# Performance work log

Hardware: AMD Instinct MI355X
Metric: run time of the kernel (lower is better)

Reference implementation:

```python
import jax, jax.numpy as jnp
import numpy as np

N0, N1, N2 = 2000, 6000, 4000
C = 128
T = 2  # conv_order
N_LAYERS = 2


def _cheb(L, x):
    """Chebyshev-style repeated application: returns [n, c, T]."""
    outs = []
    cur = x
    for _ in range(T):
        cur = L @ cur
        outs.append(cur)
    return jnp.stack(outs, axis=-1)


def _sccnn_layer(x0, x1, x2, L0, L1d, L1u, L2d, L2u, B1, B2, w0, w1, w2):
    # node space
    x_0_to_0 = jnp.concatenate([x0[..., None], _cheb(L0, x0)], -1)          # [N0,C,1+T]
    x_1_to_0 = B1 @ x1
    x_1_to_0 = jnp.concatenate([x_1_to_0[..., None], _cheb(L0, x_1_to_0)], -1)
    x_0_all = jnp.concatenate([x_0_to_0, x_1_to_0], -1)                      # [N0,C,2T+2]

    # edge space
    x_1_to_1 = jnp.concatenate([x1[..., None], _cheb(L1d, x1), _cheb(L1u, x1)], -1)  # [N1,C,2T+1]
    x_0_to_1 = B1.T @ x0
    x_0_to_1 = jnp.concatenate([x_0_to_1[..., None], _cheb(L1d, x_0_to_1)], -1)
    x_2_to_1 = B2 @ x2
    x_2_to_1 = jnp.concatenate([x_2_to_1[..., None], _cheb(L1u, x_2_to_1)], -1)
    x_1_all = jnp.concatenate([x_1_to_1, x_0_to_1, x_2_to_1], -1)            # [N1,C,4T+3]

    # face space (sc_order > 2: down+up Laplacians)
    x_2_to_2 = jnp.concatenate([x2[..., None], _cheb(L2d, x2), _cheb(L2u, x2)], -1)
    x_1_to_2 = B2.T @ x1
    x_1_to_2 = jnp.concatenate([x_1_to_2[..., None], _cheb(L2d, x_1_to_2)], -1)
    x_2_all = jnp.concatenate([x_2_to_2, x_1_to_2], -1)                      # [N2,C,3T+2]

    y0 = jnp.einsum("nik,iok->no", x_0_all, w0)
    y1 = jnp.einsum("nik,iok->no", x_1_all, w1)
    y2 = jnp.einsum("nik,iok->no", x_2_all, w2)
    return y0, y1, y2  # update_func=None


def setup_inputs() -> dict:
    key = jax.random.key(0)
    ks = jax.random.split(key, 32)
    f32 = jnp.float32
    inp = {
        "x0": jax.random.normal(ks[0], (N0, C), f32),
        "x1": jax.random.normal(ks[1], (N1, C), f32),
        "x2": jax.random.normal(ks[2], (N2, C), f32),
        # scale operators ~1/sqrt(n) so repeated application stays well-conditioned
        "L0": jax.random.normal(ks[3], (N0, N0), f32) / np.float32(N0) ** 0.5,
        "L1d": jax.random.normal(ks[4], (N1, N1), f32) / np.float32(N1) ** 0.5,
        "L1u": jax.random.normal(ks[5], (N1, N1), f32) / np.float32(N1) ** 0.5,
        "L2d": jax.random.normal(ks[6], (N2, N2), f32) / np.float32(N2) ** 0.5,
        "L2u": jax.random.normal(ks[7], (N2, N2), f32) / np.float32(N2) ** 0.5,
        "B1": jax.random.normal(ks[8], (N0, N1), f32) / np.float32(N1) ** 0.5,
        "B2": jax.random.normal(ks[9], (N1, N2), f32) / np.float32(N2) ** 0.5,
        # input linears (torch Linear: y = x @ W.T + b, W:[out,in])
        "in_w0": jax.random.normal(ks[10], (C, C), f32) * 0.05,
        "in_b0": jnp.zeros((C,), f32),
        "in_w1": jax.random.normal(ks[11], (C, C), f32) * 0.05,
        "in_b1": jnp.zeros((C,), f32),
        "in_w2": jax.random.normal(ks[12], (C, C), f32) * 0.05,
        "in_b2": jnp.zeros((C,), f32),
        # layer 0 weights: [in, out, k]
        "l0_w0": jax.random.normal(ks[13], (C, C, 2 * T + 2), f32) * 0.05,
        "l0_w1": jax.random.normal(ks[14], (C, C, 4 * T + 3), f32) * 0.05,
        "l0_w2": jax.random.normal(ks[15], (C, C, 3 * T + 2), f32) * 0.05,
        # layer 1 weights
        "l1_w0": jax.random.normal(ks[16], (C, C, 2 * T + 2), f32) * 0.05,
        "l1_w1": jax.random.normal(ks[17], (C, C, 4 * T + 3), f32) * 0.05,
        "l1_w2": jax.random.normal(ks[18], (C, C, 3 * T + 2), f32) * 0.05,
        # output linear on nodes -> 2 classes
        "out_w": jax.random.normal(ks[19], (2, C), f32) * 0.05,
        "out_b": jnp.zeros((2,), f32),
    }
    return inp


def reference(x0, x1, x2, L0, L1d, L1u, L2d, L2u, B1, B2,
              in_w0, in_b0, in_w1, in_b1, in_w2, in_b2,
              l0_w0, l0_w1, l0_w2, l1_w0, l1_w1, l1_w2,
              out_w, out_b):
    h0 = x0 @ in_w0.T + in_b0
    h1 = x1 @ in_w1.T + in_b1
    h2 = x2 @ in_w2.T + in_b2
    layer_ws = [(l0_w0, l0_w1, l0_w2), (l1_w0, l1_w1, l1_w2)]
    for w0, w1, w2 in layer_ws:
        h0, h1, h2 = _sccnn_layer(h0, h1, h2, L0, L1d, L1u, L2d, L2u, B1, B2, w0, w1, w2)
    logits = h0 @ out_w.T + out_b  # [N0, 2]
    return jax.nn.sigmoid(logits)
```

## Files before the change

### kernel.cpp

```cpp
#include <hip/hip_runtime.h>
#include <cstdint>

typedef __bf16 bf16_t;
typedef bf16_t bf16x8 __attribute__((ext_vector_type(8)));
typedef float f32x4v __attribute__((ext_vector_type(4)));
typedef float f32x16 __attribute__((ext_vector_type(16)));
typedef unsigned long long u64;

#define GLD16(gp, lp)                                                        \
  __builtin_amdgcn_global_load_lds(                                          \
      (const __attribute__((address_space(1))) unsigned int*)(gp),           \
      (__attribute__((address_space(3))) unsigned int*)(lp), 16, 0, 0)

struct GDesc {
  const void* A; const void* Ac; const void* Bt; const void* Bc; const void* bias;
  bf16_t* outN; bf16_t* outT;
  int M, N, K, lda, ldbt, ldN, ldT, bstart, nbm, aext, bext;
};
struct GBatch { const unsigned* flagp; int nd; GDesc d[6]; };

__device__ __forceinline__ int imin(int a, int b) { return a < b ? a : b; }

__global__ __launch_bounds__(256) void detect_dtype(const void* probe, unsigned* flag) {
  __shared__ int cnt;
  if (threadIdx.x == 0) cnt = 0;
  __syncthreads();
  const unsigned short* u = (const unsigned short*)probe;
  int c = 0;
  for (int i = threadIdx.x; i < 4096; i += 256) {
    int e = (u[2 * i] >> 7) & 0xFF;
    if (e >= 97 && e <= 157) c++;
  }
  atomicAdd(&cnt, c);
  __syncthreads();
  if (threadIdx.x == 0) *flag = (cnt >= 3277) ? 1u : 0u;
}

struct CvtJob { const float* src; bf16_t* dst; };
struct CvtBatch {
  const unsigned* flagp; int nj; unsigned total4;
  unsigned base[12]; CvtJob j[12];
};
__global__ __launch_bounds__(256) void cvt_f32_bf16(CvtBatch cb) {
  if (*cb.flagp != 0) return;
  const unsigned stride = gridDim.x * 256;
  for (unsigned idx = blockIdx.x * 256 + threadIdx.x; idx < cb.total4; idx += stride) {
    int ji = 0;
#pragma unroll 1
    for (int i = 1; i < cb.nj; ++i)
      if (idx >= cb.base[i]) ji = i;
    const unsigned e = idx - cb.base[ji];
    float4 v = ((const float4*)cb.j[ji].src)[e];
    union { bf16_t b[4]; uint2 u; } o;
    o.b[0] = (bf16_t)v.x; o.b[1] = (bf16_t)v.y;
    o.b[2] = (bf16_t)v.z; o.b[3] = (bf16_t)v.w;
    *(uint2*)(cb.j[ji].dst + (u64)e * 4) = o.u;
  }
}

__global__ __launch_bounds__(256) void gemm_stage(GBatch gb) {
  __shared__ __align__(16) char smem[49152];
  bf16_t* const sAb = (bf16_t*)smem;
  bf16_t* const sBb = (bf16_t*)smem + 3 * 4096;
  float* const sT = (float*)smem;

  const int bid = blockIdx.x;
  int di = 0;
#pragma unroll 1
  for (int i = 1; i < gb.nd; ++i)
    if (bid >= gb.d[i].bstart) di = i;
  const GDesc g = gb.d[di];

  const unsigned fl = *gb.flagp;
  bool a32 = false, b32 = false;
  const bf16_t* Ab; const bf16_t* Bb;
  const float* Af = (const float*)g.A;
  const float* Bf = (const float*)g.Bt;
  if (fl != 0) {
    Ab = (const bf16_t*)g.A; Bb = (const bf16_t*)g.Bt;
  } else {
    if (g.aext) { Ab = (const bf16_t*)g.Ac; a32 = (g.Ac == nullptr); }
    else Ab = (const bf16_t*)g.A;
    if (g.bext) { Bb = (const bf16_t*)g.Bc; b32 = (g.Bc == nullptr); }
    else Bb = (const bf16_t*)g.Bt;
  }

  const int t = threadIdx.x;
  const int w = t >> 6, lane = t & 63;
  const int local = bid - g.bstart;
  const int bm = local % g.nbm, bn = local / g.nbm;
  const int m0 = bm * 128, c0 = bn * 128;

  const int srow = t >> 2;
  const int sc = ((t & 3) ^ ((t >> 3) & 3)) * 8;
  const u64 eA0 = (u64)imin(m0 + srow, g.M - 1) * g.lda + sc;
  const u64 eA1 = (u64)imin(m0 + 64 + srow, g.M - 1) * g.lda + sc;
  const u64 eB0 = (u64)imin(c0 + srow, g.N - 1) * g.ldbt + sc;
  const u64 eB1 = (u64)imin(c0 + 64 + srow, g.N - 1) * g.ldbt + sc;

  const int wm = w & 1, wn = w >> 1;
  const int lrow = lane & 31, lhalf = lane >> 5;
  const int fr = (lrow >> 1) & 3;
  const int aoffb = (wm * 64 + lrow) * 32;
  const int boffb = (wn * 64 + lrow) * 32;

  f32x16 acc[2][2] = {};

  auto cvt8 = [](const float* p) {
    float4 u0 = *(const float4*)p, u1 = *(const float4*)(p + 4);
    bf16x8 r;
    r[0] = (bf16_t)u0.x; r[1] = (bf16_t)u0.y; r[2] = (bf16_t)u0.z; r[3] = (bf16_t)u0.w;
    r[4] = (bf16_t)u1.x; r[5] = (bf16_t)u1.y; r[6] = (bf16_t)u1.z; r[7] = (bf16_t)u1.w;
    return r;
  };

  auto mfma_step = [&](const bf16_t* bA, const bf16_t* bB) {
    bf16x8 af[2][2], bb[2][2];
#pragma unroll
    for (int s = 0; s < 2; ++s)
#pragma unroll
      for (int h = 0; h < 2; ++h) {
        const int sl = ((lhalf + 2 * h) ^ fr) * 8;
        af[s][h] = *(const bf16x8*)&bA[aoffb + s * 1024 + sl];
        bb[s][h] = *(const bf16x8*)&bB[boffb + s * 1024 + sl];
      }
#pragma unroll
    for (int h = 0; h < 2; ++h)
#pragma unroll
      for (int sm = 0; sm < 2; ++sm)
#pragma unroll
        for (int sn = 0; sn < 2; ++sn)
          acc[sm][sn] = __builtin_amdgcn_mfma_f32_32x32x16_bf16(
              af[sm][h], bb[sn][h], acc[sm][sn], 0, 0, 0);
  };

  auto issueP = [&](int kk, int buf) {
    const u64 kb = (u64)kk * 32;
    bf16_t* dA = sAb + buf * 4096 + w * 512;
    bf16_t* dB = sBb + buf * 4096 + w * 512;
    GLD16(Ab + eA0 + kb, dA);
    GLD16(Ab + eA1 + kb, dA + 2048);
    GLD16(Bb + eB0 + kb, dB);
    GLD16(Bb + eB1 + kb, dB + 2048);
  };

  const int kfull = g.K >> 5;
  if (!a32 && !b32) {
    issueP(0, 0);
    if (kfull > 1) {
      issueP(1, 1);
      asm volatile("s_waitcnt vmcnt(4)" ::: "memory");
    } else {
      asm volatile("s_waitcnt vmcnt(0)" ::: "memory");
    }
    __builtin_amdgcn_s_barrier();
    int cur = 0, nxt = 2;
#pragma unroll 1
    for (int kk = 0; kk < kfull; ++kk) {
      const bool pre = (kk + 2 < kfull);
      if (pre) issueP(kk + 2, nxt);
      mfma_step(sAb + cur * 4096, sBb + cur * 4096);
      if (pre) asm volatile("s_waitcnt vmcnt(4)" ::: "memory");
      else     asm volatile("s_waitcnt vmcnt(0)" ::: "memory");
      __builtin_amdgcn_s_barrier();
      cur = (cur == 2) ? 0 : cur + 1;
      nxt = (nxt == 2) ? 0 : nxt + 1;
    }
  } else {
#pragma unroll 1
    for (int kk = 0; kk < kfull; ++kk) {
      const u64 kb = (u64)kk * 32;
      if (!a32) {
        GLD16(Ab + eA0 + kb, sAb + w * 512);
        GLD16(Ab + eA1 + kb, sAb + w * 512 + 2048);
      } else {
        *(bf16x8*)(sAb + (u64)t * 8) = cvt8(Af + eA0 + kb);
        *(bf16x8*)(sAb + (u64)t * 8 + 2048) = cvt8(Af + eA1 + kb);
      }
      if (!b32) {
        GLD16(Bb + eB0 + kb, sBb + w * 512);
        GLD16(Bb + eB1 + kb, sBb + w * 512 + 2048);
      } else {
        *(bf16x8*)(sBb + (u64)t * 8) = cvt8(Bf + eB0 + kb);
        *(bf16x8*)(sBb + (u64)t * 8 + 2048) = cvt8(Bf + eB1 + kb);
      }
      __syncthreads();
      mfma_step(sAb, sBb);
      __syncthreads();
    }
  }

  if (g.K & 16) {
    const u64 k0 = (u64)(g.K & ~31);
    const int row = t >> 1;
    const int g0 = t & 1;
    const int ftl = (row >> 1) & 3;
    const u64 ea = (u64)imin(m0 + row, g.M - 1) * g.lda + k0 + g0 * 8;
    const u64 eb = (u64)imin(c0 + row, g.N - 1) * g.ldbt + k0 + g0 * 8;
    bf16x8 va, vb;
    if (!a32) va = *(const bf16x8*)(Ab + ea);
    else va = cvt8(Af + ea);
    if (!b32) vb = *(const bf16x8*)(Bb + eb);
    else vb = cvt8(Bf + eb);
    uint4 z = {0, 0, 0, 0};
    *(bf16x8*)&sAb[row * 32 + ((g0 ^ ftl) * 8)] = va;
    *(uint4*)&sAb[row * 32 + (((g0 | 2) ^ ftl) * 8)] = z;
    *(bf16x8*)&sBb[row * 32 + ((g0 ^ ftl) * 8)] = vb;
    *(uint4*)&sBb[row * 32 + (((g0 | 2) ^ ftl) * 8)] = z;
    __syncthreads();
    mfma_step(sAb, sBb);
    __syncthreads();
  }

  if (g.bias) {
#pragma unroll
    for (int sm = 0; sm < 2; ++sm)
#pragma unroll
      for (int reg = 0; reg < 16; ++reg) {
        int mg = imin(m0 + wm * 64 + sm * 32 + (reg & 3) + 8 * (reg >> 2) + 4 * lhalf,
                      g.M - 1);
        float bv = (fl == 0) ? ((const float*)g.bias)[mg]
                             : (float)((const bf16_t*)g.bias)[mg];
        acc[sm][0][reg] += bv;
        acc[sm][1][reg] += bv;
      }
  }
  if (g.outN) {
#pragma unroll
    for (int sm = 0; sm < 2; ++sm)
#pragma unroll
      for (int sn = 0; sn < 2; ++sn) {
        int cg = c0 + wn * 64 + sn * 32 + lrow;
        if (cg < g.N) {
#pragma unroll
          for (int reg = 0; reg < 16; ++reg) {
            int mg = m0 + wm * 64 + sm * 32 + (reg & 3) + 8 * (reg >> 2) + 4 * lhalf;
            if (mg < g.M) g.outN[(u64)mg * g.ldN + cg] = (bf16_t)acc[sm][sn][reg];
          }
        }
      }
  }
  if (g.outT) {
#pragma unroll
    for (int cc = 0; cc < 4; ++cc) {
      __syncthreads();
      if (wn == (cc >> 1)) {
        const int sn = cc & 1;
#pragma unroll
        for (int sm = 0; sm < 2; ++sm)
#pragma unroll
          for (int rq = 0; rq < 4; ++rq) {
            f32x4v v;
            v.x = acc[sm][sn][rq * 4 + 0];
            v.y = acc[sm][sn][rq * 4 + 1];
            v.z = acc[sm][sn][rq * 4 + 2];
            v.w = acc[sm][sn][rq * 4 + 3];
            int ml = wm * 64 + sm * 32 + 8 * rq + 4 * lhalf;
            *(f32x4v*)&sT[lrow * 132 + ml] = v;
          }
      }
      __syncthreads();
#pragma unroll
      for (int p = 0; p < 4; ++p) {
        int c = (t >> 5) + p * 8, mq = t & 31;
        f32x4v v = *(const f32x4v*)&sT[c * 132 + mq * 4];
        int cg = c0 + cc * 32 + c;
        if (cg < g.N) {
          union { bf16_t b[4]; uint2 u; } cv;
          cv.b[0] = (bf16_t)v.x; cv.b[1] = (bf16_t)v.y;
          cv.b[2] = (bf16_t)v.z; cv.b[3] = (bf16_t)v.w;
          *(uint2*)(g.outT + (u64)cg * g.ldT + m0 + mq * 4) = cv.u;
        }
      }
    }
  }
}

__global__ __launch_bounds__(256) void transpose_any(const void* in, bf16_t* out,
                                                     bf16_t* out_rm,
                                                     int Ri, int Ci, int tilesC,
                                                     const unsigned* flagp) {
  __shared__ bf16_t tile[64 * 65];
  const bool f32m = (*flagp == 0);
  const int bi = blockIdx.x / tilesC, bj = blockIdx.x % tilesC;
  const int i0 = bi * 64, j0 = bj * 64;
  const int t = threadIdx.x;
#pragma unroll
  for (int it = 0; it < 16; ++it) {
    int flidx = t + it * 256;
    int r = flidx >> 6, c = flidx & 63;
    int gi = i0 + r, gj = j0 + c;
    bf16_t v = (bf16_t)0.f;
    if (gi < Ri && gj < Ci) {
      u64 idx = (u64)gi * Ci + gj;
      v = f32m ? (bf16_t)((const float*)in)[idx] : ((const bf16_t*)in)[idx];
      if (out_rm && f32m) out_rm[idx] = v;
    }
    tile[r * 65 + c] = v;
  }
  __syncthreads();
#pragma unroll
  for (int it = 0; it < 2; ++it) {
    int flidx = t + it * 256;
    int c = flidx >> 3, rb = (flidx & 7) * 8;
    int gj = j0 + c;
    if (gj < Ci && (i0 + rb) < Ri) {
      union { bf16_t b[8]; uint4 u; } cv;
#pragma unroll
      for (int k2 = 0; k2 < 8; ++k2) cv.b[k2] = tile[(rb + k2) * 65 + c];
      *(uint4*)(out + (u64)gj * Ri + i0 + rb) = cv.u;
    }
  }
}

struct RPack {
  const void* src[3]; bf16_t* dst[3];
  int R[3], ks[3], base[3], total;
  const unsigned* flagp;
};
__global__ __launch_bounds__(256) void repack_w(RPack rp) {
  int id = blockIdx.x * 256 + threadIdx.x;
  if (id >= rp.total) return;
  const bool f32m = (*rp.flagp == 0);
  int si = 0;
  if (id >= rp.base[1]) si = 1;
  if (id >= rp.base[2]) si = 2;
  int e = id - rp.base[si];
  int R = rp.R[si], ks = rp.ks[si];
  int o = e / R, col = e - o * R;
  int k = col >> 7, i = col & 127;
  u64 sidx = ((u64)i * 128 + o) * ks + k;
  rp.dst[si][e] = f32m ? (bf16_t)((const float*)rp.src[si])[sidx]
                       : ((const bf16_t*)rp.src[si])[sidx];
}

__global__ __launch_bounds__(256) void final_head(const bf16_t* h0t, const void* ow,
                                                  const void* ob, void* out,
                                                  const unsigned* flagp) {
  int n = blockIdx.x * 256 + threadIdx.x;
  if (n >= 2000) return;
  const bool f32m = (*flagp == 0);
  float a0 = f32m ? ((const float*)ob)[0] : (float)((const bf16_t*)ob)[0];
  float a1 = f32m ? ((const float*)ob)[1] : (float)((const bf16_t*)ob)[1];
#pragma unroll 4
  for (int i = 0; i < 128; ++i) {
    float hv = (float)h0t[i * 2048 + n];
    float w0 = f32m ? ((const float*)ow)[i] : (float)((const bf16_t*)ow)[i];
    float w1 = f32m ? ((const float*)ow)[128 + i] : (float)((const bf16_t*)ow)[128 + i];
    a0 += hv * w0;
    a1 += hv * w1;
  }
  float s0 = 1.f / (1.f + __expf(-a0));
  float s1 = 1.f / (1.f + __expf(-a1));
  if (f32m) {
    ((float*)out)[n * 2 + 0] = s0;
    ((float*)out)[n * 2 + 1] = s1;
  } else {
    ((bf16_t*)out)[n * 2 + 0] = (bf16_t)s0;
    ((bf16_t*)out)[n * 2 + 1] = (bf16_t)s1;
  }
}

extern "C" void kernel_launch(void* const* d_in, const int* in_sizes, int n_in,
                              void* d_out, int out_size, void* d_ws, size_t ws_size,
                              hipStream_t stream) {
  const void *x0 = d_in[0], *x1 = d_in[1], *x2 = d_in[2];
  const void *L0 = d_in[3], *L1d = d_in[4], *L1u = d_in[5];
  const void *B1m = d_in[8];
  const void *B2m = d_in[9];
  const void *inw0 = d_in[10], *inb0 = d_in[11], *inw1 = d_in[12], *inb1 = d_in[13],
             *inw2 = d_in[14], *inb2 = d_in[15];
  const void *w0a = d_in[16], *w1a = d_in[17], *w0b = d_in[19];
  const void *outw = d_in[22], *outb = d_in[23];

  char* wsb = (char*)d_ws;
  size_t off = 0;
  auto alloc = [&](size_t elems) {
    bf16_t* p = (bf16_t*)(wsb + off);
    off = (off + elems * 2 + 255) & ~(size_t)255;
    return p;
  };
  unsigned* flagp = (unsigned*)alloc(128);
  bf16_t* B1t = alloc((size_t)6000 * 2000);
  bf16_t* h0t = alloc(128 * 2048);
  bf16_t* h1t = alloc(128 * 6016);
  bf16_t* h2t = alloc(128 * 4096);
  bf16_t* p_t = alloc(128 * 2048);
  bf16_t* q_t = alloc(128 * 6016);
  bf16_t* r_t = alloc(128 * 6016);
  bf16_t* a_t = alloc(128 * 2048);
  bf16_t* c_t = alloc(128 * 2048);
  bf16_t* e_t = alloc(128 * 6016);
  bf16_t* g_t = alloc(128 * 6016);
  bf16_t* j_t = alloc(128 * 6016);
  bf16_t* l_t = alloc(128 * 6016);
  bf16_t* sA0 = alloc((size_t)2000 * 768);
  bf16_t* sA1 = alloc((size_t)6000 * 1408);
  bf16_t* sB0 = alloc((size_t)2000 * 768);
  bf16_t* Wp0a = alloc(768 * 128);
  bf16_t* Wp1a = alloc(1408 * 128);
  bf16_t* Wp0b = alloc(768 * 128);
  bf16_t* L0c  = alloc((size_t)2000 * 2000);
  bf16_t* L1dc = alloc((size_t)6000 * 6000);
  bf16_t* L1uc = alloc((size_t)6000 * 6000);
  bf16_t* B2c  = alloc((size_t)6000 * 4000);
  bf16_t* B1rm = alloc((size_t)2000 * 6000);
  bf16_t* x0c  = alloc((size_t)2000 * 128);
  bf16_t* x1c  = alloc((size_t)6000 * 128);
  bf16_t* x2c  = alloc((size_t)4000 * 128);
  bf16_t* iw0c = alloc(128 * 128);
  bf16_t* iw1c = alloc(128 * 128);
  bf16_t* iw2c = alloc(128 * 128);

  const bool fit = off <= ws_size;
  auto C = [&](bf16_t* p) { return fit ? p : (bf16_t*)nullptr; };

  detect_dtype<<<1, 256, 0, stream>>>(L0, flagp);

  if (fit) {
    CvtBatch cb{};
    cb.flagp = flagp;
    int nj = 0; unsigned tot4 = 0;
    auto addcvt = [&](const void* src, bf16_t* dst, size_t n) {
      cb.j[nj].src = (const float*)src; cb.j[nj].dst = dst;
      cb.base[nj] = tot4; tot4 += (unsigned)(n >> 2); nj++;
    };
    addcvt(L0, L0c, (size_t)2000 * 2000);
    addcvt(L1d, L1dc, (size_t)6000 * 6000);
    addcvt(L1u, L1uc, (size_t)6000 * 6000);
    addcvt(B2m, B2c, (size_t)6000 * 4000);
    addcvt(x0, x0c, (size_t)2000 * 128);
    addcvt(x1, x1c, (size_t)6000 * 128);
    addcvt(x2, x2c, (size_t)4000 * 128);
    addcvt(inw0, iw0c, 128 * 128);
    addcvt(inw1, iw1c, 128 * 128);
    addcvt(inw2, iw2c, 128 * 128);
    cb.nj = nj; cb.total4 = tot4;
    cvt_f32_bf16<<<2048, 256, 0, stream>>>(cb);
  }

  RPack rp{};
  rp.src[0] = w0a; rp.dst[0] = Wp0a; rp.R[0] = 768;  rp.ks[0] = 6;  rp.base[0] = 0;
  rp.src[1] = w1a; rp.dst[1] = Wp1a; rp.R[1] = 1408; rp.ks[1] = 11; rp.base[1] = 98304;
  rp.src[2] = w0b; rp.dst[2] = Wp0b; rp.R[2] = 768;  rp.ks[2] = 6;  rp.base[2] = 98304 + 180224;
  rp.total = 98304 + 180224 + 98304;
  rp.flagp = flagp;
  repack_w<<<(rp.total + 255) / 256, 256, 0, stream>>>(rp);

  transpose_any<<<32 * 94, 256, 0, stream>>>(B1m, B1t, C(B1rm), 2000, 6000, 94, flagp);

  GBatch gb; int tot;
  gb.flagp = flagp;
  auto reset = [&] { gb.nd = 0; tot = 0; };
  auto add = [&](const void* A, const void* Ac, int aext,
                 const void* Bt, const void* Bc, int bext, const void* bias,
                 bf16_t* outN, int ldN, bf16_t* outT, int ldT,
                 int M, int N, int K, int lda, int ldbt) {
    GDesc& d = gb.d[gb.nd++];
    d.A = A; d.Ac = Ac; d.Bt = Bt; d.Bc = Bc; d.bias = bias;
    d.outN = outN; d.outT = outT;
    d.M = M; d.N = N; d.K = K; d.lda = lda; d.ldbt = ldbt; d.ldN = ldN; d.ldT = ldT;
    d.aext = aext; d.bext = bext;
    d.bstart = tot; d.nbm = (M + 127) >> 7;
    tot += d.nbm * ((N + 127) >> 7);
  };
  auto fire = [&] { gemm_stage<<<tot, 256, 0, stream>>>(gb); };

  reset();
  add(inw0, C(iw0c), 1, x0, C(x0c), 1, inb0, h0t, 2048, sA0, 768, 128, 2000, 128, 128, 128);
  add(inw1, C(iw1c), 1, x1, C(x1c), 1, inb1, h1t, 6016, sA1, 1408, 128, 6000, 128, 128, 128);
  add(inw2, C(iw2c), 1, x2, C(x2c), 1, inb2, h2t, 4096, nullptr, 0, 128, 4000, 128, 128, 128);
  fire();

  reset();
  add(B1m, C(B1rm), 1, h1t, nullptr, 0, nullptr, sA0 + 3 * 128, 768, p_t, 2048, 2000, 128, 6000, 6000, 6016);
  add(B1t, nullptr, 0, h0t, nullptr, 0, nullptr, sA1 + 5 * 128, 1408, q_t, 6016, 6000, 128, 2000, 2000, 2048);
  add(B2m, C(B2c), 1, h2t, nullptr, 0, nullptr, sA1 + 8 * 128, 1408, r_t, 6016, 6000, 128, 4000, 4000, 4096);
  add(L0, C(L0c), 1, h0t, nullptr, 0, nullptr, sA0 + 1 * 128, 768, a_t, 2048, 2000, 128, 2000, 2000, 2048);
  add(L1d, C(L1dc), 1, h1t, nullptr, 0, nullptr, sA1 + 1 * 128, 1408, e_t, 6016, 6000, 128, 6000, 6000, 6016);
  add(L1u, C(L1uc), 1, h1t, nullptr, 0, nullptr, sA1 + 3 * 128, 1408, g_t, 6016, 6000, 128, 6000, 6000, 6016);
  fire();

  reset();
  add(L0, C(L0c), 1, p_t, nullptr, 0, nullptr, sA0 + 4 * 128, 768, c_t, 2048, 2000, 128, 2000, 2000, 2048);
  add(L0, C(L0c), 1, a_t, nullptr, 0, nullptr, sA0 + 2 * 128, 768, nullptr, 0, 2000, 128, 2000, 2000, 2048);
  add(L1d, C(L1dc), 1, q_t, nullptr, 0, nullptr, sA1 + 6 * 128, 1408, j_t, 6016, 6000, 128, 6000, 6000, 6016);
  add(L1d, C(L1dc), 1, e_t, nullptr, 0, nullptr, sA1 + 2 * 128, 1408, nullptr, 0, 6000, 128, 6000, 6000, 6016);
  add(L1u, C(L1uc), 1, r_t, nullptr, 0, nullptr, sA1 + 9 * 128, 1408, l_t, 6016, 6000, 128, 6000, 6000, 6016);
  add(L1u, C(L1uc), 1, g_t, nullptr, 0, nullptr, sA1 + 4 * 128, 1408, nullptr, 0, 6000, 128, 6000, 6000, 6016);
  fire();

  reset();
  add(L0, C(L0c), 1, c_t, nullptr, 0, nullptr, sA0 + 5 * 128, 768, nullptr, 0, 2000, 128, 2000, 2000, 2048);
  add(L1d, C(L1dc), 1, j_t, nullptr, 0, nullptr, sA1 + 7 * 128, 1408, nullptr, 0, 6000, 128, 6000, 6000, 6016);
  add(L1u, C(L1uc), 1, l_t, nullptr, 0, nullptr, sA1 + 10 * 128, 1408, nullptr, 0, 6000, 128, 6000, 6000, 6016);
  fire();

  reset();
  add(sA0, nullptr, 0, Wp0a, nullptr, 0, nullptr, sB0, 768, h0t, 2048, 2000, 128, 768, 768, 768);
  add(sA1, nullptr, 0, Wp1a, nullptr, 0, nullptr, nullptr, 0, h1t, 6016, 6000, 128, 1408, 1408, 1408);
  fire();

  reset();
  add(B1m, C(B1rm), 1, h1t, nullptr, 0, nullptr, sB0 + 3 * 128, 768, p_t, 2048, 2000, 128, 6000, 6000, 6016);
  add(L0, C(L0c), 1, h0t, nullptr, 0, nullptr, sB0 + 1 * 128, 768, a_t, 2048, 2000, 128, 2000, 2000, 2048);
  fire();
  reset();
  add(L0, C(L0c), 1, p_t, nullptr, 0, nullptr, sB0 + 4 * 128, 768, c_t, 2048, 2000, 128, 2000, 2000, 2048);
  add(L0, C(L0c), 1, a_t, nullptr, 0, nullptr, sB0 + 2 * 128, 768, nullptr, 0, 2000, 128, 2000, 2000, 2048);
  fire();
  reset();
  add(L0, C(L0c), 1, c_t, nullptr, 0, nullptr, sB0 + 5 * 128, 768, nullptr, 0, 2000, 128, 2000, 2000, 2048);
  fire();
  reset();
  add(sB0, nullptr, 0, Wp0b, nullptr, 0, nullptr, nullptr, 0, h0t, 2048, 2000, 128, 768, 768, 768);
  fire();

  final_head<<<8, 256, 0, stream>>>(h0t, outw, outb, d_out, flagp);
}
```

Baseline: 1.050 ms.

## Add split-K GEMM with reduction kernel, deeper LDS pipeline, vectorized transpose/convert

Adds split-K to the batched GEMM stage: partial 128x128 tiles are written to an fp32 workspace and a new ksum_finalize kernel sums them and writes the normal and transposed bf16 outputs. This is meant to fill the GPU on the small, low-occupancy later stages (the layer-2 node chain and the third-hop Chebyshev products). The LDS prefetch pipeline also goes from 3 to 4 stages (64KB shared memory), the conversion kernel gets per-job block ranges instead of a per-element job search, and the transpose loads 4 elements per thread. The costs are extra launches, fp32 partial-sum traffic and larger LDS use, which may lower occupancy.

Measured after the change: 1.204 ms. 14.7% more time.

```diff
diff --git a/kernel.cpp b/kernel.cpp
--- a/kernel.cpp
+++ b/kernel.cpp
@@ -14,8 +14,8 @@
 
 struct GDesc {
   const void* A; const void* Ac; const void* Bt; const void* Bc; const void* bias;
-  bf16_t* outN; bf16_t* outT;
-  int M, N, K, lda, ldbt, ldN, ldT, bstart, nbm, aext, bext;
+  bf16_t* outN; bf16_t* outT; float* accum;
+  int M, N, K, lda, ldbt, ldN, ldT, bstart, nbm, nbn, ksplit, aext, bext;
 };
 struct GBatch { const unsigned* flagp; int nd; GDesc d[6]; };
 
@@ -38,30 +38,37 @@
 
 struct CvtJob { const float* src; bf16_t* dst; };
 struct CvtBatch {
-  const unsigned* flagp; int nj; unsigned total4;
-  unsigned base[12]; CvtJob j[12];
+  const unsigned* flagp; int nj;
+  int bb[13];
+  unsigned n4[12];
+  CvtJob j[12];
 };
 __global__ __launch_bounds__(256) void cvt_f32_bf16(CvtBatch cb) {
   if (*cb.flagp != 0) return;
-  const unsigned stride = gridDim.x * 256;
-  for (unsigned idx = blockIdx.x * 256 + threadIdx.x; idx < cb.total4; idx += stride) {
-    int ji = 0;
-#pragma unroll 1
-    for (int i = 1; i < cb.nj; ++i)
-      if (idx >= cb.base[i]) ji = i;
-    const unsigned e = idx - cb.base[ji];
-    float4 v = ((const float4*)cb.j[ji].src)[e];
+  int ji = 0;
+#pragma unroll 1
+  for (int i = 1; i < cb.nj; ++i)
+    if ((int)blockIdx.x >= cb.bb[i]) ji = i;
+  const unsigned nb = (unsigned)(cb.bb[ji + 1] - cb.bb[ji]);
+  const unsigned n4 = cb.n4[ji];
+  const float4* src = (const float4*)cb.j[ji].src;
+  bf16_t* dst = cb.j[ji].dst;
+  unsigned idx = (blockIdx.x - cb.bb[ji]) * 256 + threadIdx.x;
+  const unsigned stride = nb * 256;
+#pragma unroll 1
+  for (; idx < n4; idx += stride) {
+    float4 v = src[idx];
     union { bf16_t b[4]; uint2 u; } o;
     o.b[0] = (bf16_t)v.x; o.b[1] = (bf16_t)v.y;
     o.b[2] = (bf16_t)v.z; o.b[3] = (bf16_t)v.w;
-    *(uint2*)(cb.j[ji].dst + (u64)e * 4) = o.u;
+    *(uint2*)(dst + (u64)idx * 4) = o.u;
   }
 }
 
 __global__ __launch_bounds__(256) void gemm_stage(GBatch gb) {
-  __shared__ __align__(16) char smem[49152];
+  __shared__ __align__(16) char smem[65536];
   bf16_t* const sAb = (bf16_t*)smem;
-  bf16_t* const sBb = (bf16_t*)smem + 3 * 4096;
+  bf16_t* const sBb = (bf16_t*)smem + 4 * 4096;
   float* const sT = (float*)smem;
 
   const int bid = blockIdx.x;
@@ -88,8 +95,21 @@
   const int t = threadIdx.x;
   const int w = t >> 6, lane = t & 63;
   const int local = bid - g.bstart;
-  const int bm = local % g.nbm, bn = local / g.nbm;
+  const int bm = local % g.nbm;
+  const int rest = local / g.nbm;
+  const int bn = rest % g.nbn;
+  const int ks = rest / g.nbn;
   const int m0 = bm * 128, c0 = bn * 128;
+
+  int kbeg = 0, kend = g.K;
+  if (g.ksplit > 1) {
+    const int Kc = ((g.K + g.ksplit * 32 - 1) / (g.ksplit * 32)) * 32;
+    kbeg = ks * Kc;
+    kend = imin(g.K, kbeg + Kc);
+  }
+  const int len = kend - kbeg;
+  const int kfull = (len > 0) ? (len >> 5) : 0;
+  const bool hasTail = (g.K & 16) && (kend == g.K) && (len > 0);
 
   const int srow = t >> 2;
   const int sc = ((t & 3) ^ ((t >> 3) & 3)) * 8;
@@ -135,7 +155,7 @@
   };
 
   auto issueP = [&](int kk, int buf) {
-    const u64 kb = (u64)kk * 32;
+    const u64 kb = (u64)kbeg + (u64)kk * 32;
     bf16_t* dA = sAb + buf * 4096 + w * 512;
     bf16_t* dB = sBb + buf * 4096 + w * 512;
     GLD16(Ab + eA0 + kb, dA);
@@ -144,32 +164,29 @@
     GLD16(Bb + eB1 + kb, dB + 2048);
   };
 
-  const int kfull = g.K >> 5;
   if (!a32 && !b32) {
-    issueP(0, 0);
-    if (kfull > 1) {
-      issueP(1, 1);
-      asm volatile("s_waitcnt vmcnt(4)" ::: "memory");
-    } else {
-      asm volatile("s_waitcnt vmcnt(0)" ::: "memory");
-    }
-    __builtin_amdgcn_s_barrier();
-    int cur = 0, nxt = 2;
+    int issued = 0;
+    while (issued < kfull && issued < 3) { issueP(issued, issued & 3); ++issued; }
+    if (kfull > 0) {
+      if (issued >= 3)      asm volatile("s_waitcnt vmcnt(8)" ::: "memory");
+      else if (issued == 2) asm volatile("s_waitcnt vmcnt(4)" ::: "memory");
+      else                  asm volatile("s_waitcnt vmcnt(0)" ::: "memory");
+      __builtin_amdgcn_s_barrier();
+    }
 #pragma unroll 1
     for (int kk = 0; kk < kfull; ++kk) {
-      const bool pre = (kk + 2 < kfull);
-      if (pre) issueP(kk + 2, nxt);
-      mfma_step(sAb + cur * 4096, sBb + cur * 4096);
-      if (pre) asm volatile("s_waitcnt vmcnt(4)" ::: "memory");
-      else     asm volatile("s_waitcnt vmcnt(0)" ::: "memory");
+      if (issued < kfull) { issueP(issued, issued & 3); ++issued; }
+      mfma_step(sAb + (kk & 3) * 4096, sBb + (kk & 3) * 4096);
+      const int lead = issued - kk;
+      if (lead >= 4)      asm volatile("s_waitcnt vmcnt(8)" ::: "memory");
+      else if (lead == 3) asm volatile("s_waitcnt vmcnt(4)" ::: "memory");
+      else if (lead == 2) asm volatile("s_waitcnt vmcnt(0)" ::: "memory");
       __builtin_amdgcn_s_barrier();
-      cur = (cur == 2) ? 0 : cur + 1;
-      nxt = (nxt == 2) ? 0 : nxt + 1;
     }
   } else {
 #pragma unroll 1
     for (int kk = 0; kk < kfull; ++kk) {
-      const u64 kb = (u64)kk * 32;
+      const u64 kb = (u64)kbeg + (u64)kk * 32;
       if (!a32) {
         GLD16(Ab + eA0 + kb, sAb + w * 512);
         GLD16(Ab + eA1 + kb, sAb + w * 512 + 2048);
@@ -190,7 +207,7 @@
     }
   }
 
-  if (g.K & 16) {
+  if (hasTail) {
     const u64 k0 = (u64)(g.K & ~31);
     const int row = t >> 1;
     const int g0 = t & 1;
@@ -212,6 +229,22 @@
     __syncthreads();
   }
 
+  if (g.ksplit > 1) {
+    float* ap = g.accum + (u64)ks * (u64)g.nbm * 128 * 128 + (u64)m0 * 128;
+#pragma unroll
+    for (int sm = 0; sm < 2; ++sm)
+#pragma unroll
+      for (int sn = 0; sn < 2; ++sn) {
+        const int cg = wn * 64 + sn * 32 + lrow;
+#pragma unroll
+        for (int reg = 0; reg < 16; ++reg) {
+          const int mg = wm * 64 + sm * 32 + (reg & 3) + 8 * (reg >> 2) + 4 * lhalf;
+          ap[(u64)mg * 128 + cg] = acc[sm][sn][reg];
+        }
+      }
+    return;
+  }
+
   if (g.bias) {
 #pragma unroll
     for (int sm = 0; sm < 2; ++sm)
@@ -276,6 +309,40 @@
   }
 }
 
+struct KFJob { const float* acc; bf16_t* outN; bf16_t* outT; int M, Mpad, ldN, ldT, ksplit; };
+struct KFBatch { int nj; int base[8]; KFJob j[8]; };
+__global__ __launch_bounds__(256) void ksum_finalize(KFBatch kb) {
+  __shared__ float tile[64][132];
+  int ji = 0;
+#pragma unroll 1
+  for (int i = 1; i < kb.nj; ++i)
+    if ((int)blockIdx.x >= kb.base[i]) ji = i;
+  const KFJob j = kb.j[ji];
+  const int m0 = (blockIdx.x - kb.base[ji]) * 64;
+  const int t = threadIdx.x;
+#pragma unroll 1
+  for (int idx = t; idx < 64 * 128; idx += 256) {
+    const int m = idx >> 7, c = idx & 127;
+    float s = 0.f;
+#pragma unroll 1
+    for (int ks = 0; ks < j.ksplit; ++ks)
+      s += j.acc[((u64)ks * j.Mpad + m0 + m) * 128 + c];
+    if (j.outN && (m0 + m) < j.M) j.outN[(u64)(m0 + m) * j.ldN + c] = (bf16_t)s;
+    tile[m][c] = s;
+  }
+  if (j.outT) {
+    __syncthreads();
+#pragma unroll 1
+    for (int idx = t; idx < 128 * 8; idx += 256) {
+      const int c = idx >> 3, ch = idx & 7;
+      union { bf16_t b[8]; uint4 u; } cv;
+#pragma unroll
+      for (int r = 0; r < 8; ++r) cv.b[r] = (bf16_t)tile[ch * 8 + r][c];
+      *(uint4*)(j.outT + (u64)c * j.ldT + m0 + ch * 8) = cv.u;
+    }
+  }
+}
+
 __global__ __launch_bounds__(256) void transpose_any(const void* in, bf16_t* out,
                                                      bf16_t* out_rm,
                                                      int Ri, int Ci, int tilesC,
@@ -286,17 +353,41 @@
   const int i0 = bi * 64, j0 = bj * 64;
   const int t = threadIdx.x;
 #pragma unroll
-  for (int it = 0; it < 16; ++it) {
-    int flidx = t + it * 256;
-    int r = flidx >> 6, c = flidx & 63;
-    int gi = i0 + r, gj = j0 + c;
-    bf16_t v = (bf16_t)0.f;
+  for (int it = 0; it < 4; ++it) {
+    int r = (t >> 4) + it * 16;
+    int c4 = (t & 15) * 4;
+    int gi = i0 + r, gj = j0 + c4;
+    bf16_t v0 = (bf16_t)0.f, v1 = v0, v2 = v0, v3 = v0;
     if (gi < Ri && gj < Ci) {
-      u64 idx = (u64)gi * Ci + gj;
-      v = f32m ? (bf16_t)((const float*)in)[idx] : ((const bf16_t*)in)[idx];
-      if (out_rm && f32m) out_rm[idx] = v;
-    }
-    tile[r * 65 + c] = v;
+      u64 base = (u64)gi * Ci + gj;
+      if (gj + 3 < Ci) {
+        if (f32m) {
+          float4 v = *(const float4*)((const float*)in + base);
+          v0 = (bf16_t)v.x; v1 = (bf16_t)v.y; v2 = (bf16_t)v.z; v3 = (bf16_t)v.w;
+          if (out_rm) {
+            union { bf16_t b[4]; uint2 u; } cv;
+            cv.b[0] = v0; cv.b[1] = v1; cv.b[2] = v2; cv.b[3] = v3;
+            *(uint2*)(out_rm + base) = cv.u;
+          }
+        } else {
+          const bf16_t* p = (const bf16_t*)in + base;
+          v0 = p[0]; v1 = p[1]; v2 = p[2]; v3 = p[3];
+        }
+      } else {
+#pragma unroll
+        for (int k2 = 0; k2 < 4; ++k2) {
+          if (gj + k2 < Ci) {
+            bf16_t vv = f32m ? (bf16_t)((const float*)in)[base + k2]
+                             : ((const bf16_t*)in)[base + k2];
+            if (k2 == 0) v0 = vv; else if (k2 == 1) v1 = vv;
+            else if (k2 == 2) v2 = vv; else v3 = vv;
+            if (out_rm && f32m) out_rm[base + k2] = vv;
+          }
+        }
+      }
+    }
+    tile[r * 65 + c4 + 0] = v0; tile[r * 65 + c4 + 1] = v1;
+    tile[r * 65 + c4 + 2] = v2; tile[r * 65 + c4 + 3] = v3;
   }
   __syncthreads();
 #pragma unroll
@@ -411,6 +502,7 @@
   bf16_t* iw0c = alloc(128 * 128);
   bf16_t* iw1c = alloc(128 * 128);
   bf16_t* iw2c = alloc(128 * 128);
+  float* accPool = (float*)alloc((size_t)10 * 1024 * 1024);
 
   const bool fit = off <= ws_size;
   auto C = [&](bf16_t* p) { return fit ? p : (bf16_t*)nullptr; };
@@ -420,10 +512,11 @@
   if (fit) {
     CvtBatch cb{};
     cb.flagp = flagp;
-    int nj = 0; unsigned tot4 = 0;
+    int nj = 0;
+    u64 tot4 = 0;
     auto addcvt = [&](const void* src, bf16_t* dst, size_t n) {
       cb.j[nj].src = (const float*)src; cb.j[nj].dst = dst;
-      cb.base[nj] = tot4; tot4 += (unsigned)(n >> 2); nj++;
+      cb.n4[nj] = (unsigned)(n >> 2); tot4 += (n >> 2); nj++;
     };
     addcvt(L0, L0c, (size_t)2000 * 2000);
     addcvt(L1d, L1dc, (size_t)6000 * 6000);
@@ -435,8 +528,20 @@
     addcvt(inw0, iw0c, 128 * 128);
     addcvt(inw1, iw1c, 128 * 128);
     addcvt(inw2, iw2c, 128 * 128);
-    cb.nj = nj; cb.total4 = tot4;
-    cvt_f32_bf16<<<2048, 256, 0, stream>>>(cb);
+    cb.nj = nj;
+    const int CVTBLK = 2048;
+    int used = 0, big = 0;
+    int nb[12];
+    for (int i = 0; i < nj; ++i) {
+      nb[i] = (int)(((u64)CVTBLK * cb.n4[i]) / tot4);
+      if (nb[i] < 1) nb[i] = 1;
+      used += nb[i];
+      if (cb.n4[i] > cb.n4[big]) big = i;
+    }
+    nb[big] += CVTBLK - used;
+    cb.bb[0] = 0;
+    for (int i = 0; i < nj; ++i) cb.bb[i + 1] = cb.bb[i] + nb[i];
+    cvt_f32_bf16<<<CVTBLK, 256, 0, stream>>>(cb);
   }
 
   RPack rp{};
@@ -451,69 +556,86 @@
 
   GBatch gb; int tot;
   gb.flagp = flagp;
-  auto reset = [&] { gb.nd = 0; tot = 0; };
+  KFBatch kf; int kfblocks; float* accCur;
+  auto reset = [&] { gb.nd = 0; tot = 0; kf.nj = 0; kfblocks = 0; accCur = accPool; };
   auto add = [&](const void* A, const void* Ac, int aext,
                  const void* Bt, const void* Bc, int bext, const void* bias,
                  bf16_t* outN, int ldN, bf16_t* outT, int ldT,
-                 int M, int N, int K, int lda, int ldbt) {
+                 int M, int N, int K, int lda, int ldbt, int ksplit) {
     GDesc& d = gb.d[gb.nd++];
     d.A = A; d.Ac = Ac; d.Bt = Bt; d.Bc = Bc; d.bias = bias;
-    d.outN = outN; d.outT = outT;
+    d.outN = outN; d.outT = outT; d.accum = nullptr;
     d.M = M; d.N = N; d.K = K; d.lda = lda; d.ldbt = ldbt; d.ldN = ldN; d.ldT = ldT;
     d.aext = aext; d.bext = bext;
-    d.bstart = tot; d.nbm = (M + 127) >> 7;
-    tot += d.nbm * ((N + 127) >> 7);
+    d.nbm = (M + 127) >> 7;
+    d.nbn = (N + 127) >> 7;
+    d.ksplit = fit ? ksplit : 1;
+    if (d.ksplit > 1) {
+      d.accum = accCur;
+      accCur += (size_t)d.ksplit * d.nbm * 128 * 128;
+      KFJob& fj = kf.j[kf.nj];
+      fj.acc = d.accum; fj.outN = outN; fj.outT = outT;
+      fj.M = M; fj.Mpad = d.nbm * 128; fj.ldN = ldN; fj.ldT = ldT; fj.ksplit = d.ksplit;
+      kf.base[kf.nj] = kfblocks;
+      kfblocks += (M + 63) / 64;
+      kf.nj++;
+    }
+    d.bstart = tot;
+    tot += d.nbm * d.nbn * d.ksplit;
   };
-  auto fire = [&] { gemm_stage<<<tot, 256, 0, stream>>>(gb); };
-
-  reset();
-  add(inw0, C(iw0c), 1, x0, C(x0c), 1, inb0, h0t, 2048, sA0, 768, 128, 2000, 128, 128, 128);
-  add(inw1, C(iw1c), 1, x1, C(x1c), 1, inb1, h1t, 6016, sA1, 1408, 128, 6000, 128, 128, 128);
-  add(inw2, C(iw2c), 1, x2, C(x2c), 1, inb2, h2t, 4096, nullptr, 0, 128, 4000, 128, 128, 128);
-  fire();
-
-  reset();
-  add(B1m, C(B1rm), 1, h1t, nullptr, 0, nullptr, sA0 + 3 * 128, 768, p_t, 2048, 2000, 128, 6000, 6000, 6016);
-  add(B1t, nullptr, 0, h0t, nullptr, 0, nullptr, sA1 + 5 * 128, 1408, q_t, 6016, 6000, 128, 2000, 2000, 2048);
-  add(B2m, C(B2c), 1, h2t, nullptr, 0, nullptr, sA1 + 8 * 128, 1408, r_t, 6016, 6000, 128, 4000, 4000, 4096);
-  add(L0, C(L0c), 1, h0t, nullptr, 0, nullptr, sA0 + 1 * 128, 768, a_t, 2048, 2000, 128, 2000, 2000, 2048);
-  add(L1d, C(L1dc), 1, h1t, nullptr, 0, nullptr, sA1 + 1 * 128, 1408, e_t, 6016, 6000, 128, 6000, 6000, 6016);
-  add(L1u, C(L1uc), 1, h1t, nullptr, 0, nullptr, sA1 + 3 * 128, 1408, g_t, 6016, 6000, 128, 6000, 6000, 6016);
-  fire();
-
-  reset();
-  add(L0, C(L0c), 1, p_t, nullptr, 0, nullptr, sA0 + 4 * 128, 768, c_t, 2048, 2000, 128, 2000, 2000, 2048);
-  add(L0, C(L0c), 1, a_t, nullptr, 0, nullptr, sA0 + 2 * 128, 768, nullptr, 0, 2000, 128, 2000, 2000, 2048);
-  add(L1d, C(L1dc), 1, q_t, nullptr, 0, nullptr, sA1 + 6 * 128, 1408, j_t, 6016, 6000, 128, 6000, 6000, 6016);
-  add(L1d, C(L1dc), 1, e_t, nullptr, 0, nullptr, sA1 + 2 * 128, 1408, nullptr, 0, 6000, 128, 6000, 6000, 6016);
-  add(L1u, C(L1uc), 1, r_t, nullptr, 0, nullptr, sA1 + 9 * 128, 1408, l_t, 6016, 6000, 128, 6000, 6000, 6016);
-  add(L1u, C(L1uc), 1, g_t, nullptr, 0, nullptr, sA1 + 4 * 128, 1408, nullptr, 0, 6000, 128, 6000, 6000, 6016);
-  fire();
-
-  reset();
-  add(L0, C(L0c), 1, c_t, nullptr, 0, nullptr, sA0 + 5 * 128, 768, nullptr, 0, 2000, 128, 2000, 2000, 2048);
-  add(L1d, C(L1dc), 1, j_t, nullptr, 0, nullptr, sA1 + 7 * 128, 1408, nullptr, 0, 6000, 128, 6000, 6000, 6016);
-  add(L1u, C(L1uc), 1, l_t, nullptr, 0, nullptr, sA1 + 10 * 128, 1408, nullptr, 0, 6000, 128, 6000, 6000, 6016);
-  fire();
-
-  reset();
-  add(sA0, nullptr, 0, Wp0a, nullptr, 0, nullptr, sB0, 768, h0t, 2048, 2000, 128, 768, 768, 768);
-  add(sA1, nullptr, 0, Wp1a, nullptr, 0, nullptr, nullptr, 0, h1t, 6016, 6000, 128, 1408, 1408, 1408);
-  fire();
-
-  reset();
-  add(B1m, C(B1rm), 1, h1t, nullptr, 0, nullptr, sB0 + 3 * 128, 768, p_t, 2048, 2000, 128, 6000, 6000, 6016);
-  add(L0, C(L0c), 1, h0t, nullptr, 0, nullptr, sB0 + 1 * 128, 768, a_t, 2048, 2000, 128, 2000, 2000, 2048);
-  fire();
-  reset();
-  add(L0, C(L0c), 1, p_t, nullptr, 0, nullptr, sB0 + 4 * 128, 768, c_t, 2048, 2000, 128, 2000, 2000, 2048);
-  add(L0, C(L0c), 1, a_t, nullptr, 0, nullptr, sB0 + 2 * 128, 768, nullptr, 0, 2000, 128, 2000, 2000, 2048);
-  fire();
-  reset();
-  add(L0, C(L0c), 1, c_t, nullptr, 0, nullptr, sB0 + 5 * 128, 768, nullptr, 0, 2000, 128, 2000, 2000, 2048);
-  fire();
-  reset();
-  add(sB0, nullptr, 0, Wp0b, nullptr, 0, nullptr, nullptr, 0, h0t, 2048, 2000, 128, 768, 768, 768);
+  auto fire = [&] {
+    gemm_stage<<<tot, 256, 0, stream>>>(gb);
+    if (kf.nj) ksum_finalize<<<kfblocks, 256, 0, stream>>>(kf);
+  };
+
+  reset();
+  add(inw0, C(iw0c), 1, x0, C(x0c), 1, inb0, h0t, 2048, sA0, 768, 128, 2000, 128, 128, 128, 1);
+  add(inw1, C(iw1c), 1, x1, C(x1c), 1, inb1, h1t, 6016, sA1, 1408, 128, 6000, 128, 128, 128, 1);
+  add(inw2, C(iw2c), 1, x2, C(x2c), 1, inb2, h2t, 4096, nullptr, 0, 128, 4000, 128, 128, 128, 1);
+  fire();
+
+  reset();
+  add(B1m, C(B1rm), 1, h1t, nullptr, 0, nullptr, sA0 + 3 * 128, 768, p_t, 2048, 2000, 128, 6000, 6000, 6016, 1);
+  add(B1t, nullptr, 0, h0t, nullptr, 0, nullptr, sA1 + 5 * 128, 1408, q_t, 6016, 6000, 128, 2000, 2000, 2048, 1);
+  add(B2m, C(B2c), 1, h2t, nullptr, 0, nullptr, sA1 + 8 * 128, 1408, r_t, 6016, 6000, 128, 4000, 4000, 4096, 1);
+  add(L0, C(L0c), 1, h0t, nullptr, 0, nullptr, sA0 + 1 * 128, 768, a_t, 2048, 2000, 128, 2000, 2000, 2048, 1);
+  add(L1d, C(L1dc), 1, h1t, nullptr, 0, nullptr, sA1 + 1 * 128, 1408, e_t, 6016, 6000, 128, 6000, 6000, 6016, 1);
+  add(L1u, C(L1uc), 1, h1t, nullptr, 0, nullptr, sA1 + 3 * 128, 1408, g_t, 6016, 6000, 128, 6000, 6000, 6016, 1);
+  fire();
+
+  reset();
+  add(L0, C(L0c), 1, p_t, nullptr, 0, nullptr, sA0 + 4 * 128, 768, c_t, 2048, 2000, 128, 2000, 2000, 2048, 1);
+  add(L0, C(L0c), 1, a_t, nullptr, 0, nullptr, sA0 + 2 * 128, 768, nullptr, 0, 2000, 128, 2000, 2000, 2048, 1);
+  add(L1d, C(L1dc), 1, q_t, nullptr, 0, nullptr, sA1 + 6 * 128, 1408, j_t, 6016, 6000, 128, 6000, 6000, 6016, 1);
+  add(L1d, C(L1dc), 1, e_t, nullptr, 0, nullptr, sA1 + 2 * 128, 1408, nullptr, 0, 6000, 128, 6000, 6000, 6016, 1);
+  add(L1u, C(L1uc), 1, r_t, nullptr, 0, nullptr, sA1 + 9 * 128, 1408, l_t, 6016, 6000, 128, 6000, 6000, 6016, 1);
+  add(L1u, C(L1uc), 1, g_t, nullptr, 0, nullptr, sA1 + 4 * 128, 1408, nullptr, 0, 6000, 128, 6000, 6000, 6016, 1);
+  fire();
+
+  reset();
+  add(L0, C(L0c), 1, c_t, nullptr, 0, nullptr, sA0 + 5 * 128, 768, nullptr, 0, 2000, 128, 2000, 2000, 2048, 2);
+  add(L1d, C(L1dc), 1, j_t, nullptr, 0, nullptr, sA1 + 7 * 128, 1408, nullptr, 0, 6000, 128, 6000, 6000, 6016, 2);
+  add(L1u, C(L1uc), 1, l_t, nullptr, 0, nullptr, sA1 + 10 * 128, 1408, nullptr, 0, 6000, 128, 6000, 6000, 6016, 2);
+  fire();
+
+  reset();
+  add(sA0, nullptr, 0, Wp0a, nullptr, 0, nullptr, sB0, 768, h0t, 2048, 2000, 128, 768, 768, 768, 2);
+  add(sA1, nullptr, 0, Wp1a, nullptr, 0, nullptr, nullptr, 0, h1t, 6016, 6000, 128, 1408, 1408, 1408, 2);
+  fire();
+
+  reset();
+  add(B1m, C(B1rm), 1, h1t, nullptr, 0, nullptr, sB0 + 3 * 128, 768, p_t, 2048, 2000, 128, 6000, 6000, 6016, 12);
+  add(L0, C(L0c), 1, h0t, nullptr, 0, nullptr, sB0 + 1 * 128, 768, a_t, 2048, 2000, 128, 2000, 2000, 2048, 4);
+  fire();
+  reset();
+  add(L0, C(L0c), 1, p_t, nullptr, 0, nullptr, sB0 + 4 * 128, 768, c_t, 2048, 2000, 128, 2000, 2000, 2048, 8);
+  add(L0, C(L0c), 1, a_t, nullptr, 0, nullptr, sB0 + 2 * 128, 768, nullptr, 0, 2000, 128, 2000, 2000, 2048, 8);
+  fire();
+  reset();
+  add(L0, C(L0c), 1, c_t, nullptr, 0, nullptr, sB0 + 5 * 128, 768, nullptr, 0, 2000, 128, 2000, 2000, 2048, 8);
+  fire();
+  reset();
+  add(sB0, nullptr, 0, Wp0b, nullptr, 0, nullptr, nullptr, 0, h0t, 2048, 2000, 128, 768, 768, 768, 4);
   fire();
 
   final_head<<<8, 256, 0, stream>>>(h0t, outw, outb, d_out, flagp);
```
